# Kernel optimization log

Measured on AMD Instinct MI355X. Metric: run time of the kernel, lower is better.

Reference implementation:

```python
import jax, jax.numpy as jnp
from jax import lax
import numpy as np

B, T, F_IN, H = 64, 128, 12, 128  # batch, seq_len, input/output features, hidden


def _uinit(key, shape, fan):
    return jax.random.uniform(key, shape, jnp.float32, -1.0, 1.0) / np.float32(np.sqrt(fan))


def setup_inputs() -> dict:
    key = jax.random.key(0)
    ks = jax.random.split(key, 12)
    inp = {
        "x": jax.random.normal(ks[0], (B, T, F_IN), jnp.float32),
        # encoder LSTM (gate order i,f,g,o; b = b_ih + b_hh folded together)
        "enc_Wih": _uinit(ks[1], (4 * H, F_IN), H),
        "enc_Whh": _uinit(ks[2], (4 * H, H), H),
        "enc_b": _uinit(ks[3], (4 * H,), H),
        # decoder LSTM (input is the 12-dim teacher-forced x slice)
        "dec_Wih": _uinit(ks[4], (4 * H, F_IN), H),
        "dec_Whh": _uinit(ks[5], (4 * H, H), H),
        "dec_b": _uinit(ks[6], (4 * H,), H),
        # attention: Linear(2H -> H) with bias, then v: Linear(H -> 1, no bias)
        "attn_W": _uinit(ks[7], (H, 2 * H), 2 * H),
        "attn_b": _uinit(ks[8], (H,), 2 * H),
        "v_w": _uinit(ks[9], (H,), H),
        # output layer: Linear(2H -> F_IN)  (intended width; see notes)
        "out_W": _uinit(ks[10], (F_IN, 2 * H), 2 * H),
        "out_b": _uinit(ks[11], (F_IN,), 2 * H),
    }
    return inp


def _lstm_cell(xt, h, c, Wih, Whh, b):
    z = xt @ Wih.T + h @ Whh.T + b  # [B, 4H]
    i, f, g, o = jnp.split(z, 4, axis=-1)
    c = jax.nn.sigmoid(f) * c + jax.nn.sigmoid(i) * jnp.tanh(g)
    h = jax.nn.sigmoid(o) * jnp.tanh(c)
    return h, c


def reference(x, enc_Wih, enc_Whh, enc_b, dec_Wih, dec_Whh, dec_b,
              attn_W, attn_b, v_w, out_W, out_b):
    b_, t_, _ = x.shape
    hdim = enc_Whh.shape[1]
    xs = jnp.swapaxes(x, 0, 1)  # [T, B, F]
    h0 = jnp.zeros((b_, hdim), x.dtype)
    c0 = jnp.zeros((b_, hdim), x.dtype)

    def enc_step(carry, xt):
        h, c = carry
        h, c = _lstm_cell(xt, h, c, enc_Wih, enc_Whh, enc_b)
        return (h, c), h

    (hT, cT), enc_hs = lax.scan(enc_step, (h0, c0), xs)
    enc_out = jnp.swapaxes(enc_hs, 0, 1)  # [B, T, H]

    # split attn weight: cat(hidden, enc_out) @ W.T == hidden@W1.T + enc_out@W2.T
    W1, W2 = attn_W[:, :hdim], attn_W[:, hdim:]
    enc_proj = jnp.einsum("bth,gh->btg", enc_out, W2)  # precompute encoder side

    def dec_step(carry, xt):
        h, c = carry
        h, c = _lstm_cell(xt, h, c, dec_Wih, dec_Whh, dec_b)
        energy = jnp.tanh((h @ W1.T)[:, None, :] + enc_proj + attn_b)  # [B,T,H]
        score = jnp.einsum("bth,h->bt", energy, v_w)
        w = jax.nn.softmax(score, axis=1)  # attention over encoder time
        ctx = jnp.einsum("bt,bth->bh", w, enc_out)
        return (h, c), jnp.concatenate([h, ctx], axis=-1)  # [B, 2H]

    _, dec_ys = lax.scan(dec_step, (hT, cT), xs)
    dec_out = jnp.swapaxes(dec_ys, 0, 1)  # [B, T, 2H]
    return dec_out @ out_W.T + out_b  # [B, T, F]
```

## Files before the change

kernel.cpp:

```cpp
#include <hip/hip_runtime.h>
#include <hip/hip_bf16.h>

#define BB 64
#define TT 128
#define FIN 12
#define HH 128

#define LOG2E 1.4426950408889634f
#define TWO_LOG2E 2.8853900817779268f

__device__ __forceinline__ float fexp2(float x) { return __builtin_amdgcn_exp2f(x); }
__device__ __forceinline__ float frcp(float x)  { return __builtin_amdgcn_rcpf(x); }

__device__ __forceinline__ float tanh_f(float x) {
  return 1.0f - 2.0f * frcp(1.0f + fexp2(TWO_LOG2E * x));
}
__device__ __forceinline__ float sigm_f(float x) {
  return frcp(1.0f + fexp2(-LOG2E * x));
}

template <int CTRL>
__device__ __forceinline__ float dpp_addstage(float v) {
  int s = __builtin_amdgcn_update_dpp(0, __float_as_int(v), CTRL, 0xF, 0xF, true);
  return v + __int_as_float(s);
}
__device__ __forceinline__ float red8(float v) {
  v = dpp_addstage<0xB1>(v);
  v = dpp_addstage<0x4E>(v);
  v = dpp_addstage<0x141>(v);
  return v;
}

#define FMA4S(acc, s, v) do { \
  acc.x = fmaf((s), (v).x, acc.x); \
  acc.y = fmaf((s), (v).y, acc.y); \
  acc.z = fmaf((s), (v).z, acc.z); \
  acc.w = fmaf((s), (v).w, acc.w); } while (0)

#define ACC4(hv, wv, a) do { \
  a = fmaf((hv).x, (wv).x, a); a = fmaf((hv).y, (wv).y, a); \
  a = fmaf((hv).z, (wv).z, a); a = fmaf((hv).w, (wv).w, a); } while (0)

__device__ __forceinline__ void lstm_phase(
    const float* __restrict__ Wih, const float* __restrict__ Whh,
    const float* __restrict__ bias, float* __restrict__ Hout ,
    float* __restrict__ xs, float (*hbuf)[160], float* __restrict__ hist,
    const int tid, const int q, const int i, float& c)
{
  const int xo   = (q < 4) ? 3 * q : 0;
  const float xz = (q < 4) ? 1.0f : 0.0f;

  float4 wg[4][4];
  #pragma unroll
  for (int g = 0; g < 4; ++g)
    #pragma unroll
    for (int j = 0; j < 4; ++j)
      wg[g][j] = *(const float4*)(Whh + ((g * HH + i) * HH) + 16 * q + 4 * j);

  float wx[4][3];
  #pragma unroll
  for (int g = 0; g < 4; ++g)
    #pragma unroll
    for (int j = 0; j < 3; ++j)
      wx[g][j] = Wih[(g * HH + i) * FIN + xo + j] * xz;

  const float bi = bias[i], bf = bias[HH + i], bg = bias[2 * HH + i], bo = bias[3 * HH + i];

  int ts = 0;
  #pragma unroll 1
  for (int half = 0; half < 2; ++half) {
    #pragma unroll 1
    for (int tt = 0; tt < 64; ++tt, ++ts) {
      const int t = half * 64 + tt;
      __syncthreads();
      const float* hb = (const float*)hbuf[ts & 1] + q * 20;
      float4 h0 = *(const float4*)(hb + 0);
      float4 h1 = *(const float4*)(hb + 4);
      float4 h2 = *(const float4*)(hb + 8);
      float4 h3 = *(const float4*)(hb + 12);

      const float* xt = xs + t * FIN + xo;
      float x0 = xt[0], x1 = xt[1], x2 = xt[2];
      float ai = wx[0][0] * x0 + wx[0][1] * x1 + wx[0][2] * x2;
      float af = wx[1][0] * x0 + wx[1][1] * x1 + wx[1][2] * x2;
      float ag = wx[2][0] * x0 + wx[2][1] * x1 + wx[2][2] * x2;
      float ao = wx[3][0] * x0 + wx[3][1] * x1 + wx[3][2] * x2;

      ACC4(h0, wg[0][0], ai); ACC4(h0, wg[1][0], af); ACC4(h0, wg[2][0], ag); ACC4(h0, wg[3][0], ao);
      ACC4(h1, wg[0][1], ai); ACC4(h1, wg[1][1], af); ACC4(h1, wg[2][1], ag); ACC4(h1, wg[3][1], ao);
      ACC4(h2, wg[0][2], ai); ACC4(h2, wg[1][2], af); ACC4(h2, wg[2][2], ag); ACC4(h2, wg[3][2], ao);
      ACC4(h3, wg[0][3], ai); ACC4(h3, wg[1][3], af); ACC4(h3, wg[2][3], ag); ACC4(h3, wg[3][3], ao);

      ai = red8(ai); af = red8(af); ag = red8(ag); ao = red8(ao);

      if (q == 0) {
        float zi = sigm_f(ai + bi);
        float zf = sigm_f(af + bf);
        float zg = tanh_f(ag + bg);
        float zo = sigm_f(ao + bo);
        c = fmaf(zf, c, zi * zg);
        float hn = zo * tanh_f(c);
        hbuf[(ts + 1) & 1][(i >> 4) * 20 + (i & 15)] = hn;
        hist[tt * HH + i] = hn;
      }
    }
    __syncthreads();
    {
      float4* dst = (float4*)(Hout + (size_t)(half * 64) * HH);
      const float4* src = (const float4*)hist;
      dst[tid]        = src[tid];
      dst[tid + 1024] = src[tid + 1024];
    }
  }
}

__global__ __launch_bounds__(1024, 4) void lstm_enc_kernel(
    const float* __restrict__ x,
    const float* __restrict__ eWih, const float* __restrict__ eWhh, const float* __restrict__ eb,
    float* __restrict__ encH, float* __restrict__ decH)
{
  const int b   = blockIdx.x;
  const int tid = threadIdx.x;
  const int q   = tid & 7;
  const int i   = tid >> 3;

  __shared__ __align__(16) float xs[TT * FIN];
  __shared__ __align__(16) float hbuf[2][160];
  __shared__ __align__(16) float hist[64 * HH];

  if (tid < (TT * FIN / 4))
    ((float4*)xs)[tid] = ((const float4*)(x + (size_t)b * TT * FIN))[tid];
  if (tid < 320) ((float*)hbuf)[tid] = 0.0f;
  float c = 0.0f;

  lstm_phase(eWih, eWhh, eb, encH + (size_t)b * TT * HH, xs, hbuf, hist, tid, q, i, c);

  if (q == 0) decH[(size_t)b * TT * HH + i] = c;
}

__global__ __launch_bounds__(1024, 4) void lstm_dec_p_kernel(
    const float* __restrict__ x,
    const float* __restrict__ dWih, const float* __restrict__ dWhh, const float* __restrict__ db,
    const float* __restrict__ attnW, const float* __restrict__ outW,
    const float* __restrict__ encH,
    float* __restrict__ decH, float* __restrict__ Pbuf, float* __restrict__ y2buf)
{
  __shared__ __align__(16) float smem[12416];
  const int tid = threadIdx.x;

  if (blockIdx.x < 64) {
    const int b = blockIdx.x;
    const int q = tid & 7;
    const int i = tid >> 3;
    float* xs           = smem;
    float (*hbuf)[160]  = (float(*)[160])(smem + 1536);
    float* hist         = smem + 1856;

    if (tid < (TT * FIN / 4))
      ((float4*)xs)[tid] = ((const float4*)(x + (size_t)b * TT * FIN))[tid];
    if (tid < 128) {
      float hv = encH[((size_t)b * TT + 127) * HH + tid];
      hbuf[0][(tid >> 4) * 20 + (tid & 15)] = hv;
    }
    float c = 0.0f;
    if (q == 0) c = decH[(size_t)b * TT * HH + i];

    lstm_phase(dWih, dWhh, db, decH + (size_t)b * TT * HH, xs, hbuf, hist, tid, q, i, c);
  } else if (blockIdx.x < 192) {
    const int pb = blockIdx.x - 64;
    const int b  = pb & 63;
    const int r0 = (pb >> 6) * 64;
    float* WT = smem;
    float* Xt = smem + 4224;

    const float* X = encH + ((size_t)b * TT + r0) * HH;
    ((float4*)Xt)[tid]        = ((const float4*)X)[tid];
    ((float4*)Xt)[tid + 1024] = ((const float4*)X)[tid + 1024];

    const float* W = attnW + HH;
    const int hq = tid & 31, rr = tid >> 5;
    const int h0 = 4 * hq;

    float4 acc0 = make_float4(0.f, 0.f, 0.f, 0.f);
    float4 acc1 = acc0;

    #pragma unroll 1
    for (int kb = 0; kb < 4; ++kb) {
      __syncthreads();
      {
        int h = tid >> 3, koff = (tid & 7) * 4;
        float4 v = *(const float4*)(W + h * 256 + kb * 32 + koff);
        WT[(koff + 0) * 132 + h] = v.x;
        WT[(koff + 1) * 132 + h] = v.y;
        WT[(koff + 2) * 132 + h] = v.z;
        WT[(koff + 3) * 132 + h] = v.w;
      }
      __syncthreads();
      const float* xr0 = Xt + (2 * rr) * 128 + kb * 32;
      const float* xr1 = xr0 + 128;
      #pragma unroll
      for (int k4 = 0; k4 < 32; k4 += 4) {
        float4 xa = *(const float4*)(xr0 + k4);
        float4 xb = *(const float4*)(xr1 + k4);
        float4 w0 = *(const float4*)&WT[(k4 + 0) * 132 + h0];
        float4 w1 = *(const float4*)&WT[(k4 + 1) * 132 + h0];
        float4 w2 = *(const float4*)&WT[(k4 + 2) * 132 + h0];
        float4 w3 = *(const float4*)&WT[(k4 + 3) * 132 + h0];
        FMA4S(acc0, xa.x, w0); FMA4S(acc0, xa.y, w1);
        FMA4S(acc0, xa.z, w2); FMA4S(acc0, xa.w, w3);
        FMA4S(acc1, xb.x, w0); FMA4S(acc1, xb.y, w1);
        FMA4S(acc1, xb.z, w2); FMA4S(acc1, xb.w, w3);
      }
    }
    acc0.x = fexp2(TWO_LOG2E * acc0.x); acc0.y = fexp2(TWO_LOG2E * acc0.y);
    acc0.z = fexp2(TWO_LOG2E * acc0.z); acc0.w = fexp2(TWO_LOG2E * acc0.w);
    acc1.x = fexp2(TWO_LOG2E * acc1.x); acc1.y = fexp2(TWO_LOG2E * acc1.y);
    acc1.z = fexp2(TWO_LOG2E * acc1.z); acc1.w = fexp2(TWO_LOG2E * acc1.w);
    float* O = Pbuf + ((size_t)b * TT + r0) * HH;
    *(float4*)(O + (2 * rr) * 128 + h0)     = acc0;
    *(float4*)(O + (2 * rr + 1) * 128 + h0) = acc1;
  } else if (y2buf) {
    const int b = blockIdx.x - 192;
    float* w2l = smem;
    if (tid < 384) {
      int f = tid >> 5, k = (tid & 31) * 4;
      float4 wv = *(const float4*)(outW + f * 256 + 128 + k);
      *(float4*)&w2l[f * 132 + k] = wv;
    }
    __syncthreads();
    for (int j = tid; j < TT * 12; j += 1024) {
      int t = j / 12, f = j - 12 * t;
      const float* er = encH + ((size_t)b * TT + t) * HH;
      const float* wr = w2l + f * 132;
      float a = 0.f;
      #pragma unroll 8
      for (int k = 0; k < 32; ++k) {
        float4 ev = *(const float4*)(er + 4 * k);
        float4 wv = *(const float4*)(wr + 4 * k);
        ACC4(ev, wv, a);
      }
      y2buf[b * (TT * 16) + t * 16 + f] = a;
    }
  }
}

__global__ __launch_bounds__(256, 2) void projA_kernel(
    const float* __restrict__ decH, const float* __restrict__ attnW,
    const float* __restrict__ attnb, float* __restrict__ Abuf)
{
  const int b  = blockIdx.x & 63;
  const int r0 = (blockIdx.x >> 6) * 16;
  const int tid = threadIdx.x;

  __shared__ __align__(16) float WT[64 * 128];
  __shared__ __align__(16) float Xt[16 * 128];

  const float* X = decH + ((size_t)b * TT + r0) * HH;
  const float* W = attnW;

  ((float4*)Xt)[tid]       = ((const float4*)X)[tid];
  ((float4*)Xt)[256 + tid] = ((const float4*)X)[256 + tid];

  const int hq = tid & 31, rr = tid >> 5;
  const int h0 = 4 * hq;

  float4 acc0 = *(const float4*)(attnb + h0);
  float4 acc1 = acc0;

  for (int kb = 0; kb < 2; ++kb) {
    __syncthreads();
    {
      int h = tid >> 1, koff = (tid & 1) * 32;
      #pragma unroll
      for (int j = 0; j < 8; ++j) {
        float4 v = *(const float4*)(W + h * 256 + kb * 64 + koff + 4 * j);
        int kp = koff + 4 * j;
        WT[(kp + 0) * 128 + h] = v.x;
        WT[(kp + 1) * 128 + h] = v.y;
        WT[(kp + 2) * 128 + h] = v.z;
        WT[(kp + 3) * 128 + h] = v.w;
      }
    }
    __syncthreads();
    const float* xr0 = Xt + (2 * rr) * 128 + kb * 64;
    const float* xr1 = xr0 + 128;
    #pragma unroll
    for (int k4 = 0; k4 < 64; k4 += 4) {
      float4 xa = *(const float4*)(xr0 + k4);
      float4 xb = *(const float4*)(xr1 + k4);
      float4 w0 = *(const float4*)&WT[(k4 + 0) * 128 + h0];
      float4 w1 = *(const float4*)&WT[(k4 + 1) * 128 + h0];
      float4 w2 = *(const float4*)&WT[(k4 + 2) * 128 + h0];
      float4 w3 = *(const float4*)&WT[(k4 + 3) * 128 + h0];
      FMA4S(acc0, xa.x, w0); FMA4S(acc0, xa.y, w1);
      FMA4S(acc0, xa.z, w2); FMA4S(acc0, xa.w, w3);
      FMA4S(acc1, xb.x, w0); FMA4S(acc1, xb.y, w1);
      FMA4S(acc1, xb.z, w2); FMA4S(acc1, xb.w, w3);
    }
  }
  acc0.x = fexp2(TWO_LOG2E * acc0.x); acc0.y = fexp2(TWO_LOG2E * acc0.y);
  acc0.z = fexp2(TWO_LOG2E * acc0.z); acc0.w = fexp2(TWO_LOG2E * acc0.w);
  acc1.x = fexp2(TWO_LOG2E * acc1.x); acc1.y = fexp2(TWO_LOG2E * acc1.y);
  acc1.z = fexp2(TWO_LOG2E * acc1.z); acc1.w = fexp2(TWO_LOG2E * acc1.w);
  float* O = Abuf + ((size_t)b * TT + r0) * HH;
  *(float4*)(O + (2 * rr) * 128 + h0)     = acc0;
  *(float4*)(O + (2 * rr + 1) * 128 + h0) = acc1;
}

#define AST 132
#define Y2ST 20

__global__ __launch_bounds__(1024, 4) void attn_fused2_kernel(
    const float* __restrict__ decH, const float* __restrict__ Pbuf,
    const float* __restrict__ y2buf,
    const float* __restrict__ attnW, const float* __restrict__ attnb,
    const float* __restrict__ vw, const float* __restrict__ outW,
    const float* __restrict__ outb, float* __restrict__ out)
{
  const int b  = blockIdx.x >> 2;
  const int s0 = (blockIdx.x & 2) * 16 + (blockIdx.x & 1) * 32 * 2;
  const int s0p = (blockIdx.x & 3) * 32;
  const int tid = threadIdx.x;

  __shared__ __align__(16) float buf[128 * 128];
  __shared__ __align__(16) float w1t[64 * 132];
  __shared__ __align__(16) float a_lds[32 * AST];
  __shared__ __align__(16) float sc[32 * AST];
  __shared__ __align__(16) float dh[32 * 128];
  __shared__ __align__(16) float y2s[TT * Y2ST];
  __shared__ __align__(16) float vl[HH];

  (void)s0;
  ((float4*)dh)[tid] = ((const float4*)(decH + ((size_t)b * TT + s0p) * HH))[tid];
  if (tid < 32) ((float4*)vl)[tid] = ((const float4*)vw)[tid];
  if (tid < 512) {
    float4 v = ((const float4*)(y2buf + (size_t)b * (TT * 16)))[tid];
    int t = tid >> 2, g = (tid & 3) * 4;
    *(float4*)&y2s[t * Y2ST + g] = v;
  }
  #pragma unroll
  for (int i = 0; i < 4; ++i) {
    int flat = i * 4096 + tid * 4;
    int tp = flat >> 7;
    int h0f = flat & 127;
    float4 v = *(const float4*)(Pbuf + ((size_t)b * TT + tp) * HH + h0f);
    int hf = tp >> 6, tpl = tp & 63, tq = tpl >> 2, tr = tpl & 3;
    int base = hf * 64 + tr;
    buf[(h0f + 0) * 128 + base + 4 * ((tq ^ ((h0f + 0) >> 2)) & 15)] = v.x;
    buf[(h0f + 1) * 128 + base + 4 * ((tq ^ ((h0f + 1) >> 2)) & 15)] = v.y;
    buf[(h0f + 2) * 128 + base + 4 * ((tq ^ ((h0f + 2) >> 2)) & 15)] = v.z;
    buf[(h0f + 3) * 128 + base + 4 * ((tq ^ ((h0f + 3) >> 2)) & 15)] = v.w;
  }

  {
    const int hq = tid & 31, rr = (tid >> 5) & 15;
    const int h0 = 4 * hq;
    float4 acc0 = *(const float4*)(attnb + h0);
    float4 acc1 = acc0;
    #pragma unroll 1
    for (int kb = 0; kb < 2; ++kb) {
      __syncthreads();
      {
        int h = tid >> 3, koff = (tid & 7) * 8;
        #pragma unroll
        for (int j = 0; j < 2; ++j) {
          float4 v = *(const float4*)(attnW + h * 256 + kb * 64 + koff + 4 * j);
          int kp = koff + 4 * j;
          w1t[(kp + 0) * 132 + h] = v.x;
          w1t[(kp + 1) * 132 + h] = v.y;
          w1t[(kp + 2) * 132 + h] = v.z;
          w1t[(kp + 3) * 132 + h] = v.w;
        }
      }
      __syncthreads();
      if (tid < 512) {
        const float* xr0 = dh + (2 * rr) * 128 + kb * 64;
        const float* xr1 = xr0 + 128;
        #pragma unroll
        for (int k4 = 0; k4 < 64; k4 += 4) {
          float4 xa = *(const float4*)(xr0 + k4);
          float4 xb = *(const float4*)(xr1 + k4);
          float4 w0 = *(const float4*)&w1t[(k4 + 0) * 132 + h0];
          float4 w1 = *(const float4*)&w1t[(k4 + 1) * 132 + h0];
          float4 w2 = *(const float4*)&w1t[(k4 + 2) * 132 + h0];
          float4 w3 = *(const float4*)&w1t[(k4 + 3) * 132 + h0];
          FMA4S(acc0, xa.x, w0); FMA4S(acc0, xa.y, w1);
          FMA4S(acc0, xa.z, w2); FMA4S(acc0, xa.w, w3);
          FMA4S(acc1, xb.x, w0); FMA4S(acc1, xb.y, w1);
          FMA4S(acc1, xb.z, w2); FMA4S(acc1, xb.w, w3);
        }
      }
    }
    if (tid < 512) {
      acc0.x = fexp2(TWO_LOG2E * acc0.x); acc0.y = fexp2(TWO_LOG2E * acc0.y);
      acc0.z = fexp2(TWO_LOG2E * acc0.z); acc0.w = fexp2(TWO_LOG2E * acc0.w);
      acc1.x = fexp2(TWO_LOG2E * acc1.x); acc1.y = fexp2(TWO_LOG2E * acc1.y);
      acc1.z = fexp2(TWO_LOG2E * acc1.z); acc1.w = fexp2(TWO_LOG2E * acc1.w);
      *(float4*)&a_lds[(2 * rr) * AST + h0]     = acc0;
      *(float4*)&a_lds[(2 * rr + 1) * AST + h0] = acc1;
    }
  }
  __syncthreads();

  const int es  = tid >> 5;
  const int ehf = (tid >> 4) & 1;
  const int euq = tid & 15;
  float4 acc = make_float4(0.f, 0.f, 0.f, 0.f);
  {
    const float* earow = a_lds + es * AST;
    #pragma unroll 4
    for (int h = 0; h < 128; h += 4) {
      float4 ea = *(const float4*)&earow[h];
      float4 va = *(const float4*)&vl[h];
      const int xoff = ehf * 64 + 4 * ((euq ^ ((h >> 2) & 15)) & 15);
      float4 p0 = *(const float4*)&buf[(h + 0) * 128 + xoff];
      float4 p1 = *(const float4*)&buf[(h + 1) * 128 + xoff];
      float4 p2 = *(const float4*)&buf[(h + 2) * 128 + xoff];
      float4 p3 = *(const float4*)&buf[(h + 3) * 128 + xoff];
      acc.x = fmaf(va.x, frcp(fmaf(ea.x, p0.x, 1.f)), acc.x);
      acc.y = fmaf(va.x, frcp(fmaf(ea.x, p0.y, 1.f)), acc.y);
      acc.z = fmaf(va.x, frcp(fmaf(ea.x, p0.z, 1.f)), acc.z);
      acc.w = fmaf(va.x, frcp(fmaf(ea.x, p0.w, 1.f)), acc.w);
      acc.x = fmaf(va.y, frcp(fmaf(ea.y, p1.x, 1.f)), acc.x);
      acc.y = fmaf(va.y, frcp(fmaf(ea.y, p1.y, 1.f)), acc.y);
      acc.z = fmaf(va.y, frcp(fmaf(ea.y, p1.z, 1.f)), acc.z);
      acc.w = fmaf(va.y, frcp(fmaf(ea.y, p1.w, 1.f)), acc.w);
      acc.x = fmaf(va.z, frcp(fmaf(ea.z, p2.x, 1.f)), acc.x);
      acc.y = fmaf(va.z, frcp(fmaf(ea.z, p2.y, 1.f)), acc.y);
      acc.z = fmaf(va.z, frcp(fmaf(ea.z, p2.z, 1.f)), acc.z);
      acc.w = fmaf(va.z, frcp(fmaf(ea.z, p2.w, 1.f)), acc.w);
      acc.x = fmaf(va.w, frcp(fmaf(ea.w, p3.x, 1.f)), acc.x);
      acc.y = fmaf(va.w, frcp(fmaf(ea.w, p3.y, 1.f)), acc.y);
      acc.z = fmaf(va.w, frcp(fmaf(ea.w, p3.z, 1.f)), acc.z);
      acc.w = fmaf(va.w, frcp(fmaf(ea.w, p3.w, 1.f)), acc.w);
    }
    acc.x = -2.f * acc.x; acc.y = -2.f * acc.y;
    acc.z = -2.f * acc.z; acc.w = -2.f * acc.w;
  }

  {
    float mx = fmaxf(fmaxf(acc.x, acc.y), fmaxf(acc.z, acc.w));
    #pragma unroll
    for (int msk = 1; msk <= 16; msk <<= 1) mx = fmaxf(mx, __shfl_xor(mx, msk, 64));
    float4 e;
    e.x = fexp2(LOG2E * (acc.x - mx));
    e.y = fexp2(LOG2E * (acc.y - mx));
    e.z = fexp2(LOG2E * (acc.z - mx));
    e.w = fexp2(LOG2E * (acc.w - mx));
    float sm = (e.x + e.y) + (e.z + e.w);
    #pragma unroll
    for (int msk = 1; msk <= 16; msk <<= 1) sm += __shfl_xor(sm, msk, 64);
    float r = frcp(sm);
    e.x *= r; e.y *= r; e.z *= r; e.w *= r;
    *(float4*)&sc[es * AST + ehf * 64 + 4 * euq] = e;
  }
  __syncthreads();

  if (tid < 384) {
    int s = tid / 12, f = tid - 12 * (tid / 12);
    float acco = outb[f];
    const float4* w4 = (const float4*)(outW + f * 256);
    const float4* d4 = (const float4*)(dh + s * 128);
    #pragma unroll
    for (int k = 0; k < 32; ++k) {
      float4 wv = w4[k], dv = d4[k];
      acco = fmaf(wv.x, dv.x, acco); acco = fmaf(wv.y, dv.y, acco);
      acco = fmaf(wv.z, dv.z, acco); acco = fmaf(wv.w, dv.w, acco);
    }
    const float* wrow = sc + s * AST;
    #pragma unroll 8
    for (int t = 0; t < TT; ++t)
      acco = fmaf(wrow[t], y2s[t * Y2ST + f], acco);
    out[((size_t)b * TT + s0p + s) * FIN + f] = acco;
  }
}

__global__ __launch_bounds__(512, 2) void attn_kernel_fb(
    const float* __restrict__ encH, const float* __restrict__ decH,
    const float* __restrict__ Pbuf, const float* __restrict__ Abuf,
    const float* __restrict__ vw, const float* __restrict__ outW,
    const float* __restrict__ outb, float* __restrict__ out)
{
  const int b  = blockIdx.x >> 3;
  const int s0 = (blockIdx.x & 7) * 16;
  const int tid = threadIdx.x;

  __shared__ __align__(16) float buf[64 * 128];
  __shared__ __align__(16) float a_lds[16 * AST];
  __shared__ __align__(16) float sc[16 * AST];
  __shared__ __align__(16) float dh[16 * 128];
  __shared__ __align__(16) float vl[HH];
  __shared__ __align__(16) float y2s[TT * Y2ST];
  __shared__ __align__(16) float w2l[12 * AST];

  ((float4*)dh)[tid] = ((const float4*)(decH + ((size_t)b * TT + s0) * HH))[tid];
  if (tid < 32) ((float4*)vl)[tid] = ((const float4*)vw)[tid];
  {
    int r = tid >> 5, c4 = (tid & 31) * 4;
    float4 av = *(const float4*)(Abuf + ((size_t)b * TT + s0 + r) * HH + c4);
    *(float4*)&a_lds[r * AST + c4] = av;
  }
  if (tid < 384) {
    int f = tid >> 5, k = (tid & 31) * 4;
    float4 wv = *(const float4*)(outW + f * 256 + 128 + k);
    *(float4*)&w2l[f * AST + k] = wv;
  }

  const int u  = tid & 31;
  const int sl = tid >> 5;
  const int uq = u & 15;
  const int uh = u >> 4;

  for (int half = 0; half < 2; ++half) {
    const int tbase = half * 64;
    __syncthreads();
    #pragma unroll
    for (int i = 0; i < 4; ++i) {
      int flat = i * 2048 + tid * 4;
      int tp = flat >> 7;
      int h0 = flat & 127;
      float4 v = *(const float4*)(Pbuf + ((size_t)b * TT + tbase + tp) * HH + h0);
      int tq = tp >> 2, tr = tp & 3;
      buf[(h0 + 0) * 64 + 4 * ((tq ^ ((h0 + 0) >> 2)) & 15) + tr] = v.x;
      buf[(h0 + 1) * 64 + 4 * ((tq ^ ((h0 + 1) >> 2)) & 15) + tr] = v.y;
      buf[(h0 + 2) * 64 + 4 * ((tq ^ ((h0 + 2) >> 2)) & 15) + tr] = v.z;
      buf[(h0 + 3) * 64 + 4 * ((tq ^ ((h0 + 3) >> 2)) & 15) + tr] = v.w;
    }
    __syncthreads();
    float4 acc = make_float4(0.f, 0.f, 0.f, 0.f);
    const float* earow = a_lds + sl * AST;
    #pragma unroll 4
    for (int hh = 0; hh < 64; hh += 4) {
      const int h = uh * 64 + hh;
      float4 ea = *(const float4*)&earow[h];
      float4 va = *(const float4*)&vl[h];
      const int xoff = 4 * ((uq ^ ((h >> 2) & 15)) & 15);
      float4 p0 = *(const float4*)&buf[(h + 0) * 64 + xoff];
      float4 p1 = *(const float4*)&buf[(h + 1) * 64 + xoff];
      float4 p2 = *(const float4*)&buf[(h + 2) * 64 + xoff];
      float4 p3 = *(const float4*)&buf[(h + 3) * 64 + xoff];
      acc.x = fmaf(va.x, frcp(fmaf(ea.x, p0.x, 1.f)), acc.x);
      acc.y = fmaf(va.x, frcp(fmaf(ea.x, p0.y, 1.f)), acc.y);
      acc.z = fmaf(va.x, frcp(fmaf(ea.x, p0.z, 1.f)), acc.z);
      acc.w = fmaf(va.x, frcp(fmaf(ea.x, p0.w, 1.f)), acc.w);
      acc.x = fmaf(va.y, frcp(fmaf(ea.y, p1.x, 1.f)), acc.x);
      acc.y = fmaf(va.y, frcp(fmaf(ea.y, p1.y, 1.f)), acc.y);
      acc.z = fmaf(va.y, frcp(fmaf(ea.y, p1.z, 1.f)), acc.z);
      acc.w = fmaf(va.y, frcp(fmaf(ea.y, p1.w, 1.f)), acc.w);
      acc.x = fmaf(va.z, frcp(fmaf(ea.z, p2.x, 1.f)), acc.x);
      acc.y = fmaf(va.z, frcp(fmaf(ea.z, p2.y, 1.f)), acc.y);
      acc.z = fmaf(va.z, frcp(fmaf(ea.z, p2.z, 1.f)), acc.z);
      acc.w = fmaf(va.z, frcp(fmaf(ea.z, p2.w, 1.f)), acc.w);
      acc.x = fmaf(va.w, frcp(fmaf(ea.w, p3.x, 1.f)), acc.x);
      acc.y = fmaf(va.w, frcp(fmaf(ea.w, p3.y, 1.f)), acc.y);
      acc.z = fmaf(va.w, frcp(fmaf(ea.w, p3.z, 1.f)), acc.z);
      acc.w = fmaf(va.w, frcp(fmaf(ea.w, p3.w, 1.f)), acc.w);
    }
    acc.x += __shfl_xor(acc.x, 16, 64);
    acc.y += __shfl_xor(acc.y, 16, 64);
    acc.z += __shfl_xor(acc.z, 16, 64);
    acc.w += __shfl_xor(acc.w, 16, 64);
    if (uh == 0) {
      float4 o;
      o.x = -2.f * acc.x; o.y = -2.f * acc.y;
      o.z = -2.f * acc.z; o.w = -2.f * acc.w;
      *(float4*)&sc[sl * AST + tbase + 4 * uq] = o;
    }
  }
  __syncthreads();

  {
    float4 sv = *(const float4*)&sc[sl * AST + 4 * u];
    float mx = fmaxf(fmaxf(sv.x, sv.y), fmaxf(sv.z, sv.w));
    #pragma unroll
    for (int msk = 1; msk <= 16; msk <<= 1) mx = fmaxf(mx, __shfl_xor(mx, msk, 64));
    float4 e;
    e.x = fexp2(LOG2E * (sv.x - mx));
    e.y = fexp2(LOG2E * (sv.y - mx));
    e.z = fexp2(LOG2E * (sv.z - mx));
    e.w = fexp2(LOG2E * (sv.w - mx));
    float sm = (e.x + e.y) + (e.z + e.w);
    #pragma unroll
    for (int msk = 1; msk <= 16; msk <<= 1) sm += __shfl_xor(sm, msk, 64);
    float r = frcp(sm);
    e.x *= r; e.y *= r; e.z *= r; e.w *= r;
    *(float4*)&sc[sl * AST + 4 * u] = e;
  }

  for (int half = 0; half < 2; ++half) {
    const int tbase = half * 64;
    __syncthreads();
    #pragma unroll
    for (int i = 0; i < 4; ++i) {
      int flat = i * 2048 + tid * 4;
      int tp = flat >> 7;
      int hh0 = flat & 127;
      *(float4*)&buf[tp * 128 + hh0] =
          *(const float4*)(encH + ((size_t)b * TT + tbase + tp) * HH + hh0);
    }
    __syncthreads();
    {
      int j = tid;
      int t = j / 12, f = j - 12 * t;
      float a = 0.f;
      const float* br = buf + t * 128;
      const float* wr = w2l + f * AST;
      #pragma unroll 8
      for (int k = 0; k < 32; ++k) {
        float4 bv = *(const float4*)(br + 4 * k);
        float4 wv = *(const float4*)(wr + 4 * k);
        ACC4(bv, wv, a);
      }
      y2s[(tbase + t) * Y2ST + f] = a;
      if (tid < 256) {
        int j2 = tid + 512;
        int t2 = j2 / 12, f2 = j2 - 12 * t2;
        float a2 = 0.f;
        const float* br2 = buf + t2 * 128;
        const float* wr2 = w2l + f2 * AST;
        #pragma unroll 8
        for (int k = 0; k < 32; ++k) {
          float4 bv = *(const float4*)(br2 + 4 * k);
          float4 wv = *(const float4*)(wr2 + 4 * k);
          ACC4(bv, wv, a2);
        }
        y2s[(tbase + t2) * Y2ST + f2] = a2;
      }
    }
  }
  __syncthreads();

  if (tid < 192) {
    int s = tid / 12, f = tid - 12 * (tid / 12);
    float acc = outb[f];
    const float4* w4 = (const float4*)(outW + f * 256);
    const float4* d4 = (const float4*)(dh + s * 128);
    #pragma unroll
    for (int k = 0; k < 32; ++k) {
      float4 wv = w4[k], dv = d4[k];
      acc = fmaf(wv.x, dv.x, acc); acc = fmaf(wv.y, dv.y, acc);
      acc = fmaf(wv.z, dv.z, acc); acc = fmaf(wv.w, dv.w, acc);
    }
    const float* wrow = sc + s * AST;
    #pragma unroll 8
    for (int t = 0; t < TT; ++t)
      acc = fmaf(wrow[t], y2s[t * Y2ST + f], acc);
    out[((size_t)b * TT + s0 + s) * FIN + f] = acc;
  }
}

extern "C" void kernel_launch(void* const* d_in, const int* in_sizes, int n_in,
                              void* d_out, int out_size, void* d_ws, size_t ws_size,
                              hipStream_t stream)
{
  const float* x     = (const float*)d_in[0];
  const float* eWih  = (const float*)d_in[1];
  const float* eWhh  = (const float*)d_in[2];
  const float* eb    = (const float*)d_in[3];
  const float* dWih  = (const float*)d_in[4];
  const float* dWhh  = (const float*)d_in[5];
  const float* db    = (const float*)d_in[6];
  const float* attnW = (const float*)d_in[7];
  const float* attnb = (const float*)d_in[8];
  const float* vw    = (const float*)d_in[9];
  const float* outW  = (const float*)d_in[10];
  const float* outb  = (const float*)d_in[11];
  float* out = (float*)d_out;

  float* ws   = (float*)d_ws;
  const size_t SEG = (size_t)BB * TT * HH;
  float* encH = ws;
  float* decH = ws + SEG;
  float* Pbuf = ws + 2 * SEG;
  float* Abuf = ws + 3 * SEG;
  float* y2buf = ws + 4 * SEG;

  const size_t need_bytes = (4 * SEG + (size_t)BB * TT * 16) * sizeof(float);
  const bool have_y2 = ws_size >= need_bytes;

  lstm_enc_kernel<<<64, 1024, 0, stream>>>(x, eWih, eWhh, eb, encH, decH);
  if (have_y2) {
    lstm_dec_p_kernel<<<256, 1024, 0, stream>>>(x, dWih, dWhh, db, attnW, outW,
                                                encH, decH, Pbuf, y2buf);
    attn_fused2_kernel<<<256, 1024, 0, stream>>>(decH, Pbuf, y2buf, attnW, attnb,
                                                 vw, outW, outb, out);
  } else {
    lstm_dec_p_kernel<<<192, 1024, 0, stream>>>(x, dWih, dWhh, db, attnW, outW,
                                                encH, decH, Pbuf, nullptr);
    projA_kernel<<<512, 256, 0, stream>>>(decH, attnW, attnb, Abuf);
    attn_kernel_fb<<<512, 512, 0, stream>>>(encH, decH, Pbuf, Abuf,
                                            vw, outW, outb, out);
  }
}
```

Baseline: 314.8 us.

## Split fused attention kernel into energy/softmax and output-projection kernels

```diff
diff --git a/kernel.cpp b/kernel.cpp
--- a/kernel.cpp
+++ b/kernel.cpp
@@ -310,34 +310,23 @@
 #define AST 132
 #define Y2ST 20
 
-__global__ __launch_bounds__(1024, 4) void attn_fused2_kernel(
+__global__ __launch_bounds__(1024, 4) void attn_energy_kernel(
     const float* __restrict__ decH, const float* __restrict__ Pbuf,
-    const float* __restrict__ y2buf,
     const float* __restrict__ attnW, const float* __restrict__ attnb,
-    const float* __restrict__ vw, const float* __restrict__ outW,
-    const float* __restrict__ outb, float* __restrict__ out)
+    const float* __restrict__ vw, float* __restrict__ scbuf)
 {
-  const int b  = blockIdx.x >> 2;
-  const int s0 = (blockIdx.x & 2) * 16 + (blockIdx.x & 1) * 32 * 2;
-  const int s0p = (blockIdx.x & 3) * 32;
+  const int b   = blockIdx.x >> 2;
+  const int s0  = (blockIdx.x & 3) * 32;
   const int tid = threadIdx.x;
 
   __shared__ __align__(16) float buf[128 * 128];
   __shared__ __align__(16) float w1t[64 * 132];
   __shared__ __align__(16) float a_lds[32 * AST];
-  __shared__ __align__(16) float sc[32 * AST];
   __shared__ __align__(16) float dh[32 * 128];
-  __shared__ __align__(16) float y2s[TT * Y2ST];
   __shared__ __align__(16) float vl[HH];
 
-  (void)s0;
-  ((float4*)dh)[tid] = ((const float4*)(decH + ((size_t)b * TT + s0p) * HH))[tid];
+  ((float4*)dh)[tid] = ((const float4*)(decH + ((size_t)b * TT + s0) * HH))[tid];
   if (tid < 32) ((float4*)vl)[tid] = ((const float4*)vw)[tid];
-  if (tid < 512) {
-    float4 v = ((const float4*)(y2buf + (size_t)b * (TT * 16)))[tid];
-    int t = tid >> 2, g = (tid & 3) * 4;
-    *(float4*)&y2s[t * Y2ST + g] = v;
-  }
   #pragma unroll
   for (int i = 0; i < 4; ++i) {
     int flat = i * 4096 + tid * 4;
@@ -452,26 +441,58 @@
     for (int msk = 1; msk <= 16; msk <<= 1) sm += __shfl_xor(sm, msk, 64);
     float r = frcp(sm);
     e.x *= r; e.y *= r; e.z *= r; e.w *= r;
-    *(float4*)&sc[es * AST + ehf * 64 + 4 * euq] = e;
+    *(float4*)&scbuf[((size_t)b * TT + s0 + es) * TT + ehf * 64 + 4 * euq] = e;
+  }
+}
+
+__global__ __launch_bounds__(512, 2) void attn_out_kernel(
+    const float* __restrict__ decH, const float* __restrict__ scbuf,
+    const float* __restrict__ y2buf, const float* __restrict__ outW,
+    const float* __restrict__ outb, float* __restrict__ out)
+{
+  const int b   = blockIdx.x >> 2;
+  const int s0  = (blockIdx.x & 3) * 32;
+  const int tid = threadIdx.x;
+
+  __shared__ __align__(16) float dh[32 * 128];
+  __shared__ __align__(16) float scl[32 * AST];
+  __shared__ __align__(16) float y2s[TT * Y2ST];
+
+  ((float4*)dh)[tid]       = ((const float4*)(decH + ((size_t)b * TT + s0) * HH))[tid];
+  ((float4*)dh)[tid + 512] = ((const float4*)(decH + ((size_t)b * TT + s0) * HH))[tid + 512];
+  {
+    const float4* src = (const float4*)(scbuf + ((size_t)b * TT + s0) * TT);
+    #pragma unroll
+    for (int j = 0; j < 2; ++j) {
+      int idx = tid + j * 512;
+      float4 v = src[idx];
+      int r = idx >> 5, c4 = (idx & 31) * 4;
+      *(float4*)&scl[r * AST + c4] = v;
+    }
+  }
+  {
+    float4 v = ((const float4*)(y2buf + (size_t)b * (TT * 16)))[tid];
+    int t = tid >> 2, g = (tid & 3) * 4;
+    *(float4*)&y2s[t * Y2ST + g] = v;
   }
   __syncthreads();
 
   if (tid < 384) {
     int s = tid / 12, f = tid - 12 * (tid / 12);
-    float acco = outb[f];
+    float acc = outb[f];
     const float4* w4 = (const float4*)(outW + f * 256);
     const float4* d4 = (const float4*)(dh + s * 128);
     #pragma unroll
     for (int k = 0; k < 32; ++k) {
       float4 wv = w4[k], dv = d4[k];
-      acco = fmaf(wv.x, dv.x, acco); acco = fmaf(wv.y, dv.y, acco);
-      acco = fmaf(wv.z, dv.z, acco); acco = fmaf(wv.w, dv.w, acco);
-    }
-    const float* wrow = sc + s * AST;
+      acc = fmaf(wv.x, dv.x, acc); acc = fmaf(wv.y, dv.y, acc);
+      acc = fmaf(wv.z, dv.z, acc); acc = fmaf(wv.w, dv.w, acc);
+    }
+    const float* wrow = scl + s * AST;
     #pragma unroll 8
     for (int t = 0; t < TT; ++t)
-      acco = fmaf(wrow[t], y2s[t * Y2ST + f], acco);
-    out[((size_t)b * TT + s0p + s) * FIN + f] = acco;
+      acc = fmaf(wrow[t], y2s[t * Y2ST + f], acc);
+    out[((size_t)b * TT + s0 + s) * FIN + f] = acc;
   }
 }
 
@@ -673,6 +694,7 @@
   float* decH = ws + SEG;
   float* Pbuf = ws + 2 * SEG;
   float* Abuf = ws + 3 * SEG;
+  float* scbuf = Abuf;
   float* y2buf = ws + 4 * SEG;
 
   const size_t need_bytes = (4 * SEG + (size_t)BB * TT * 16) * sizeof(float);
@@ -682,8 +704,8 @@
   if (have_y2) {
     lstm_dec_p_kernel<<<256, 1024, 0, stream>>>(x, dWih, dWhh, db, attnW, outW,
                                                 encH, decH, Pbuf, y2buf);
-    attn_fused2_kernel<<<256, 1024, 0, stream>>>(decH, Pbuf, y2buf, attnW, attnb,
-                                                 vw, outW, outb, out);
+    attn_energy_kernel<<<256, 1024, 0, stream>>>(decH, Pbuf, attnW, attnb, vw, scbuf);
+    attn_out_kernel<<<256, 512, 0, stream>>>(decH, scbuf, y2buf, outW, outb, out);
   } else {
     lstm_dec_p_kernel<<<192, 1024, 0, stream>>>(x, dWih, dWhh, db, attnW, outW,
                                                 encH, decH, Pbuf, nullptr);
```

New measurement: 315.5 us. No clear change (+0.2%).
